# Performance work log

Hardware: AMD Instinct MI355X
Metric: run time of the kernel (lower is better)

The kernel has to match this reference:

```python
import jax, jax.numpy as jnp
import numpy as np

HEADS = 16
KEY_SIZE = 64
SIZE_PER_HEAD = 64
D_MODEL = 1024
OUT_DIM = HEADS * SIZE_PER_HEAD
NEG_BIG = 1e10


def setup_inputs() -> dict:
    key = jax.random.key(0)
    ks = jax.random.split(key, 8)
    B, S = 4, 2048
    q = jax.random.normal(ks[0], (B, S, D_MODEL), dtype=jnp.float32)
    k = jax.random.normal(ks[1], (B, S, D_MODEL), dtype=jnp.float32)
    v = jax.random.normal(ks[2], (B, S, D_MODEL), dtype=jnp.float32)
    # binary masks (1 = keep), as floats like the Keras layer expects
    v_mask = (jax.random.uniform(ks[3], (B, S)) > 0.1).astype(jnp.float32)
    q_mask = (jax.random.uniform(ks[4], (B, S)) > 0.1).astype(jnp.float32)
    sc = 1.0 / np.sqrt(D_MODEL)
    Wq = jax.random.normal(ks[5], (D_MODEL, HEADS * KEY_SIZE), dtype=jnp.float32) * sc
    Wk = jax.random.normal(ks[6], (D_MODEL, HEADS * KEY_SIZE), dtype=jnp.float32) * sc
    Wv = jax.random.normal(ks[7], (D_MODEL, OUT_DIM), dtype=jnp.float32) * sc
    return {"q": q, "k": k, "v": v, "v_mask": v_mask, "q_mask": q_mask,
            "Wq": Wq, "Wk": Wk, "Wv": Wv}


def reference(q, k, v, v_mask, q_mask, Wq, Wk, Wv):
    B, Sq, _ = q.shape
    Sk = k.shape[1]
    # projections -> [B, H, S, d]
    qw = (q @ Wq).reshape(B, Sq, HEADS, KEY_SIZE).transpose(0, 2, 1, 3)
    kw = (k @ Wk).reshape(B, Sk, HEADS, KEY_SIZE).transpose(0, 2, 1, 3)
    vw = (v @ Wv).reshape(B, Sk, HEADS, SIZE_PER_HEAD).transpose(0, 2, 1, 3)
    # scaled scores [B, H, Sq, Sk]
    a = jnp.einsum('bhqd,bhkd->bhqk', qw, kw) / np.sqrt(KEY_SIZE).astype(np.float32)
    # additive key-side mask (v_mask broadcasts over heads and query axis)
    a = a - (1.0 - v_mask[:, None, None, :]) * NEG_BIG
    # causal (mask_right): subtract big value on strictly upper triangle
    causal = jnp.triu(jnp.ones((Sq, Sk), dtype=a.dtype), k=1) * NEG_BIG
    a = a - causal[None, None]
    a = jax.nn.softmax(a, axis=-1)
    o = jnp.einsum('bhqk,bhkd->bhqd', a, vw)
    o = o.transpose(0, 2, 1, 3).reshape(B, Sq, OUT_DIM)
    # multiplicative query-side mask
    o = o * q_mask[:, :, None]
    return o
```

## Files before the change

kernel.cpp:

```cpp
#include <hip/hip_runtime.h>
#include <hip/hip_bf16.h>

typedef __bf16 bf16x8 __attribute__((ext_vector_type(8)));
typedef float f32x4 __attribute__((ext_vector_type(4)));
typedef unsigned int u32;

#define MFMA16(a, b, c) __builtin_amdgcn_mfma_f32_16x16x32_bf16(a, b, c, 0, 0, 0)

static __device__ __forceinline__ unsigned short f2b(float f) {
    __hip_bfloat16 b = __float2bfloat16(f);
    return __builtin_bit_cast(unsigned short, b);
}
static __device__ __forceinline__ float b2f(unsigned short u) {
    u32 v = ((u32)u) << 16;
    return __builtin_bit_cast(float, v);
}
static __device__ __forceinline__ unsigned short f2b_trunc(float f) {
    return (unsigned short)(__builtin_bit_cast(u32, f) >> 16);
}
static __device__ __forceinline__ void glds16(const void* g, void* l) {
    __builtin_amdgcn_global_load_lds((const __attribute__((address_space(1))) u32*)g,
                                     (__attribute__((address_space(3))) u32*)l, 16, 0, 0);
}

__global__ __launch_bounds__(256) void cvt_kernel(const float* __restrict__ src,
                                                  unsigned short* __restrict__ dst) {
    const size_t i = ((size_t)blockIdx.x * 256 + threadIdx.x) * 8;
    float4 a = *(const float4*)(src + i);
    float4 b = *(const float4*)(src + i + 4);
    ushort4 u0 = { f2b(a.x), f2b(a.y), f2b(a.z), f2b(a.w) };
    ushort4 u1 = { f2b(b.x), f2b(b.y), f2b(b.z), f2b(b.w) };
    *(ushort4*)(dst + i) = u0;
    *(ushort4*)(dst + i + 4) = u1;
}

__global__ void wt_kernel(const float* __restrict__ W0, const float* __restrict__ W1,
                          const float* __restrict__ W2, unsigned short* __restrict__ T0,
                          unsigned short* __restrict__ T1, unsigned short* __restrict__ T2) {
    const float* W = blockIdx.z == 0 ? W0 : (blockIdx.z == 1 ? W1 : W2);
    unsigned short* T = blockIdx.z == 0 ? T0 : (blockIdx.z == 1 ? T1 : T2);
    __shared__ float tile[32][33];
    const int n0 = blockIdx.x * 32, k0 = blockIdx.y * 32;
    const int tx = threadIdx.x, ty = threadIdx.y;
#pragma unroll
    for (int i = 0; i < 4; i++)
        tile[ty + 8 * i][tx] = W[(size_t)(k0 + ty + 8 * i) * 1024 + n0 + tx];
    __syncthreads();
#pragma unroll
    for (int i = 0; i < 4; i++)
        T[(size_t)(n0 + ty + 8 * i) * 1024 + k0 + tx] = f2b(tile[tx][ty + 8 * i]);
}

__global__ __launch_bounds__(256) void proj_kernel(const unsigned short* __restrict__ A,
        const unsigned short* __restrict__ Wt, unsigned short* __restrict__ dst,
        const int vmode) {
    __shared__ unsigned short smem[17408];
    unsigned short* As = smem;
    unsigned short* Bs = smem + 4096;
    const int m0 = blockIdx.y * 128, n0 = blockIdx.x * 128;
    const int tid = threadIdx.x;
    const int w = tid >> 6, lane = tid & 63, quad = lane >> 4, l16 = lane & 15;
    const int wr = (w >> 1) * 64, wc = (w & 1) * 64;
    f32x4 acc[4][4] = {};
    for (int kb = 0; kb < 32; kb++) {
        const int k0 = kb * 32;
        __syncthreads();
#pragma unroll
        for (int i = 0; i < 2; i++) {
            int idx = tid + i * 256;
            int row = idx >> 2, col = (idx & 3) * 8;
            glds16(A + (size_t)(m0 + row) * 1024 + k0 + col, &As[idx * 8]);
            glds16(Wt + (size_t)(n0 + row) * 1024 + k0 + col, &Bs[idx * 8]);
        }
        __syncthreads();
        bf16x8 af[4], bf[4];
#pragma unroll
        for (int mt = 0; mt < 4; mt++) af[mt] = *(const bf16x8*)&As[(wr + mt * 16 + l16) * 32 + quad * 8];
#pragma unroll
        for (int nt = 0; nt < 4; nt++) bf[nt] = *(const bf16x8*)&Bs[(wc + nt * 16 + l16) * 32 + quad * 8];
#pragma unroll
        for (int mt = 0; mt < 4; mt++)
#pragma unroll
            for (int nt = 0; nt < 4; nt++)
                acc[mt][nt] = MFMA16(af[mt], bf[nt], acc[mt][nt]);
    }
    __syncthreads();
    unsigned short* Tw = smem + w * 4352;
    if (vmode == 0) {
#pragma unroll
        for (int mt = 0; mt < 4; mt++)
#pragma unroll
            for (int nt = 0; nt < 4; nt++)
#pragma unroll
                for (int r = 0; r < 4; r++)
                    Tw[(mt * 16 + quad * 4 + r) * 68 + nt * 16 + l16] = f2b(acc[mt][nt][r]);
    } else {
#pragma unroll
        for (int mt = 0; mt < 4; mt++)
#pragma unroll
            for (int nt = 0; nt < 4; nt++)
#pragma unroll
                for (int r = 0; r < 4; r++)
                    Tw[(nt * 16 + l16) * 68 + mt * 16 + quad * 4 + r] = f2b(acc[mt][nt][r]);
    }
    const int gr0 = m0 + wr, gc0 = n0 + wc;
    const int b = gr0 >> 11, s0 = gr0 & 2047, h = gc0 >> 6;
    if (vmode == 0) {
        const size_t obase = (size_t)(b * 16 + h) * 2048;
#pragma unroll
        for (int j = 0; j < 16; j++) {
            int row = j * 4 + quad;
            uint2 val = *(const uint2*)&Tw[row * 68 + l16 * 4];
            *(uint2*)(dst + (obase + s0 + row) * 64 + l16 * 4) = val;
        }
    } else {
        const size_t vbase = (size_t)(b * 16 + h) * 64 * 2048;
#pragma unroll
        for (int j = 0; j < 16; j++) {
            int row = j * 4 + quad;
            uint2 val = *(const uint2*)&Tw[row * 68 + l16 * 4];
            *(uint2*)(dst + vbase + (size_t)row * 2048 + s0 + l16 * 4) = val;
        }
    }
}

__global__ __launch_bounds__(256) void attn_kernel(
        const unsigned short* __restrict__ Qp, const unsigned short* __restrict__ Kp,
        const unsigned short* __restrict__ Vt, const float* __restrict__ vmask,
        const float* __restrict__ qmask, float* __restrict__ out) {
    __shared__ unsigned short Ks[4096];
    __shared__ unsigned short Vts[4096];
    __shared__ unsigned short Ps[4096];
    __shared__ float Vmb[2048];
    const int bh = blockIdx.y, b = bh >> 4, h = bh & 15;
    const int tid = threadIdx.x;
    const int w = tid >> 6, lane = tid & 63, quad = lane >> 4, l16 = lane & 15;
    const size_t base = (size_t)bh * 2048 * 64;
    const float C1 = 0.18033688f;
    const float C0 = -11.54156036f;
    const float CM = -1.44269504e10f;
    for (int i = tid; i < 2048; i += 256)
        Vmb[i] = (vmask[b * 2048 + i] != 0.f) ? C0 : (C0 + CM);

    for (int pass = 0; pass < 2; pass++) {
        const int qt = pass ? 31 - blockIdx.x : blockIdx.x;
        const int q0 = qt * 64;
        bf16x8 qa[2];
#pragma unroll
        for (int ks = 0; ks < 2; ks++)
            qa[ks] = *(const bf16x8*)(Qp + base +
                (size_t)(q0 + w * 16 + l16) * 64 + ks * 32 + quad * 8);
        f32x4 o[4] = {};
        float lsum[4] = {};
        const int qrow = q0 + w * 16 + quad * 4;

        for (int kt = 0; kt <= qt; kt++) {
            __syncthreads();
#pragma unroll
            for (int i = 0; i < 2; i++) {
                int idx = tid + i * 256;
                int chunk = idx & 3, row = (idx >> 2) & 63, panel = idx >> 8;
                glds16(Kp + base + (size_t)(kt * 64 + row) * 64 + panel * 32 + chunk * 8, &Ks[idx * 8]);
                glds16(Vt + base + (size_t)row * 2048 + kt * 64 + panel * 32 + chunk * 8, &Vts[idx * 8]);
            }
            __syncthreads();

            f32x4 s[4];
#pragma unroll
            for (int nt = 0; nt < 4; nt++) {
                bf16x8 kf0 = *(const bf16x8*)&Ks[(nt * 16 + l16) * 32 + quad * 8];
                bf16x8 kf1 = *(const bf16x8*)&Ks[2048 + (nt * 16 + l16) * 32 + quad * 8];
                f32x4 z = {};
                z = MFMA16(qa[0], kf0, z);
                z = MFMA16(qa[1], kf1, z);
                s[nt] = z;
            }
#pragma unroll
            for (int nt = 0; nt < 4; nt++) {
                const int kv = kt * 64 + nt * 16 + l16;
                const float cb = Vmb[kv];
#pragma unroll
                for (int r = 0; r < 4; r++) {
                    float p = __builtin_amdgcn_exp2f(s[nt][r] * C1 + cb);
                    p = (kv > qrow + r) ? 0.f : p;
                    lsum[r] += p;
                    Ps[(nt >> 1) * 2048 + (w * 16 + quad * 4 + r) * 32 + (nt & 1) * 16 + l16] = f2b_trunc(p);
                }
            }
#pragma unroll
            for (int k2 = 0; k2 < 2; k2++) {
                bf16x8 pa = *(const bf16x8*)&Ps[k2 * 2048 + (w * 16 + l16) * 32 + quad * 8];
#pragma unroll
                for (int dt = 0; dt < 4; dt++) {
                    bf16x8 vb = *(const bf16x8*)&Vts[k2 * 2048 + (dt * 16 + l16) * 32 + quad * 8];
                    o[dt] = MFMA16(pa, vb, o[dt]);
                }
            }
        }
        float l[4];
#pragma unroll
        for (int r = 0; r < 4; r++) {
            float t = lsum[r];
#pragma unroll
            for (int off = 1; off < 16; off <<= 1) t += __shfl_xor(t, off);
            l[r] = t;
        }
        bool deg = (l[0] == 0.f) | (l[1] == 0.f) | (l[2] == 0.f) | (l[3] == 0.f);
        if (__any((int)deg)) {
#pragma unroll
            for (int r = 0; r < 4; r++)
                if (l[r] == 0.f) {
                    const int qr = qrow + r;
                    float cnt = 0.f;
                    float oacc[4] = {0.f, 0.f, 0.f, 0.f};
                    for (int kv = 0; kv < 2048; kv++) {
                        bool keep = (kv <= qr) || (vmask[b * 2048 + kv] != 0.f);
                        if (keep) {
                            cnt += 1.f;
#pragma unroll
                            for (int dt = 0; dt < 4; dt++)
                                oacc[dt] += b2f(Vt[base + (size_t)(dt * 16 + l16) * 2048 + kv]);
                        }
                    }
                    l[r] = cnt;
#pragma unroll
                    for (int dt = 0; dt < 4; dt++) o[dt][r] = oacc[dt];
                }
        }
#pragma unroll
        for (int r = 0; r < 4; r++) {
            int q = qrow + r;
            float sc = qmask[b * 2048 + q] / l[r];
#pragma unroll
            for (int dt = 0; dt < 4; dt++)
                out[(size_t)(b * 2048 + q) * 1024 + h * 64 + dt * 16 + l16] = o[dt][r] * sc;
        }
    }
}

extern "C" void kernel_launch(void* const* d_in, const int* in_sizes, int n_in,
                              void* d_out, int out_size, void* d_ws, size_t ws_size,
                              hipStream_t stream) {
    const float* q  = (const float*)d_in[0];
    const float* k  = (const float*)d_in[1];
    const float* v  = (const float*)d_in[2];
    const float* vm = (const float*)d_in[3];
    const float* qm = (const float*)d_in[4];
    const float* Wq = (const float*)d_in[5];
    const float* Wk = (const float*)d_in[6];
    const float* Wv = (const float*)d_in[7];
    float* out = (float*)d_out;

    unsigned short* ws  = (unsigned short*)d_ws;
    unsigned short* Wtq = ws;
    unsigned short* Wtk = Wtq + (1u << 20);
    unsigned short* Wtv = Wtk + (1u << 20);
    unsigned short* Qp  = Wtv + (1u << 20);
    unsigned short* Kp  = Qp + (1u << 23);
    unsigned short* Vtp = Kp + (1u << 23);
    unsigned short* Acvt = (unsigned short*)d_out;

    wt_kernel<<<dim3(32, 32, 3), dim3(32, 8), 0, stream>>>(Wq, Wk, Wv, Wtq, Wtk, Wtv);
    cvt_kernel<<<4096, 256, 0, stream>>>(q, Acvt);
    proj_kernel<<<dim3(8, 64), 256, 0, stream>>>(Acvt, Wtq, Qp, 0);
    cvt_kernel<<<4096, 256, 0, stream>>>(k, Acvt);
    proj_kernel<<<dim3(8, 64), 256, 0, stream>>>(Acvt, Wtk, Kp, 0);
    cvt_kernel<<<4096, 256, 0, stream>>>(v, Acvt);
    proj_kernel<<<dim3(8, 64), 256, 0, stream>>>(Acvt, Wtv, Vtp, 1);
    attn_kernel<<<dim3(16, 64), 256, 0, stream>>>(Qp, Kp, Vtp, vm, qm, out);
}
```

Measured before the change: 329.8 us.

## Batch Q/K projections, deepen GEMM K-tile, keep P in registers in attention

Q and K conversion and projection are batched into single launches with a z/y grid dimension, and the projection GEMM loads a 64-wide K slab per barrier pair, halving barrier count. Attention computes S transposed so the probabilities land directly in the MFMA A-operand layout, removing the LDS round trip for P. The causal mask is applied only on the diagonal tile, and K/V load addresses are precomputed. Grid axes are swapped so blocks of the same head are adjacent. The cost is more LDS per projection block and a dependence on the MFMA register layout being correct.

```diff
diff --git a/kernel.cpp b/kernel.cpp
--- a/kernel.cpp
+++ b/kernel.cpp
@@ -4,6 +4,7 @@
 typedef __bf16 bf16x8 __attribute__((ext_vector_type(8)));
 typedef float f32x4 __attribute__((ext_vector_type(4)));
 typedef unsigned int u32;
+typedef u32 u32x4 __attribute__((ext_vector_type(4)));
 
 #define MFMA16(a, b, c) __builtin_amdgcn_mfma_f32_16x16x32_bf16(a, b, c, 0, 0, 0)
 
@@ -15,16 +16,19 @@
     u32 v = ((u32)u) << 16;
     return __builtin_bit_cast(float, v);
 }
-static __device__ __forceinline__ unsigned short f2b_trunc(float f) {
-    return (unsigned short)(__builtin_bit_cast(u32, f) >> 16);
+static __device__ __forceinline__ u32 pk2(float lo, float hi) {
+    return (__builtin_bit_cast(u32, lo) >> 16) | (__builtin_bit_cast(u32, hi) & 0xFFFF0000u);
 }
 static __device__ __forceinline__ void glds16(const void* g, void* l) {
     __builtin_amdgcn_global_load_lds((const __attribute__((address_space(1))) u32*)g,
                                      (__attribute__((address_space(3))) u32*)l, 16, 0, 0);
 }
 
-__global__ __launch_bounds__(256) void cvt_kernel(const float* __restrict__ src,
-                                                  unsigned short* __restrict__ dst) {
+__global__ __launch_bounds__(256) void cvt2_kernel(const float* __restrict__ s0,
+        const float* __restrict__ s1, unsigned short* __restrict__ d0,
+        unsigned short* __restrict__ d1) {
+    const float* src = blockIdx.y ? s1 : s0;
+    unsigned short* dst = blockIdx.y ? d1 : d0;
     const size_t i = ((size_t)blockIdx.x * 256 + threadIdx.x) * 8;
     float4 a = *(const float4*)(src + i);
     float4 b = *(const float4*)(src + i + 4);
@@ -51,38 +55,54 @@
         T[(size_t)(n0 + ty + 8 * i) * 1024 + k0 + tx] = f2b(tile[tx][ty + 8 * i]);
 }
 
-__global__ __launch_bounds__(256) void proj_kernel(const unsigned short* __restrict__ A,
-        const unsigned short* __restrict__ Wt, unsigned short* __restrict__ dst,
-        const int vmode) {
+__global__ __launch_bounds__(256) void proj_kernel(
+        const unsigned short* __restrict__ A0, const unsigned short* __restrict__ A1,
+        const unsigned short* __restrict__ W0, const unsigned short* __restrict__ W1,
+        unsigned short* __restrict__ D0, unsigned short* __restrict__ D1, const int vmode) {
     __shared__ unsigned short smem[17408];
     unsigned short* As = smem;
-    unsigned short* Bs = smem + 4096;
-    const int m0 = blockIdx.y * 128, n0 = blockIdx.x * 128;
+    unsigned short* Bs = smem + 8192;
+    const unsigned short* A  = blockIdx.z ? A1 : A0;
+    const unsigned short* Wt = blockIdx.z ? W1 : W0;
+    unsigned short* dst      = blockIdx.z ? D1 : D0;
+    const int m0 = blockIdx.x * 128, n0 = blockIdx.y * 128;
     const int tid = threadIdx.x;
     const int w = tid >> 6, lane = tid & 63, quad = lane >> 4, l16 = lane & 15;
     const int wr = (w >> 1) * 64, wc = (w & 1) * 64;
+    const unsigned short* ap[4];
+    const unsigned short* bp[4];
+#pragma unroll
+    for (int i = 0; i < 4; i++) {
+        int idx = tid + i * 256;
+        int row = (idx >> 2) & 127, ch = (idx >> 9) * 4 + (idx & 3);
+        ap[i] = A + (size_t)(m0 + row) * 1024 + ch * 8;
+        bp[i] = Wt + (size_t)(n0 + row) * 1024 + ch * 8;
+    }
     f32x4 acc[4][4] = {};
-    for (int kb = 0; kb < 32; kb++) {
-        const int k0 = kb * 32;
+    for (int kb = 0; kb < 16; kb++) {
         __syncthreads();
 #pragma unroll
-        for (int i = 0; i < 2; i++) {
-            int idx = tid + i * 256;
-            int row = idx >> 2, col = (idx & 3) * 8;
-            glds16(A + (size_t)(m0 + row) * 1024 + k0 + col, &As[idx * 8]);
-            glds16(Wt + (size_t)(n0 + row) * 1024 + k0 + col, &Bs[idx * 8]);
+        for (int i = 0; i < 4; i++) {
+            glds16(ap[i], &As[(tid + i * 256) * 8]);
+            glds16(bp[i], &Bs[(tid + i * 256) * 8]);
+            ap[i] += 64; bp[i] += 64;
         }
         __syncthreads();
-        bf16x8 af[4], bf[4];
-#pragma unroll
-        for (int mt = 0; mt < 4; mt++) af[mt] = *(const bf16x8*)&As[(wr + mt * 16 + l16) * 32 + quad * 8];
-#pragma unroll
-        for (int nt = 0; nt < 4; nt++) bf[nt] = *(const bf16x8*)&Bs[(wc + nt * 16 + l16) * 32 + quad * 8];
-#pragma unroll
-        for (int mt = 0; mt < 4; mt++)
+#pragma unroll
+        for (int kp = 0; kp < 2; kp++) {
+            bf16x8 af[4], bf[4];
+#pragma unroll
+            for (int mt = 0; mt < 4; mt++)
+                af[mt] = *(const bf16x8*)&As[kp * 4096 + (wr + mt * 16 + l16) * 32 + quad * 8];
 #pragma unroll
             for (int nt = 0; nt < 4; nt++)
-                acc[mt][nt] = MFMA16(af[mt], bf[nt], acc[mt][nt]);
+                bf[nt] = *(const bf16x8*)&Bs[kp * 4096 + (wc + nt * 16 + l16) * 32 + quad * 8];
+#pragma unroll
+            for (int mt = 0; mt < 4; mt++)
+#pragma unroll
+                for (int nt = 0; nt < 4; nt++)
+                    acc[mt][nt] = MFMA16(af[mt], bf[nt], acc[mt][nt]);
+        }
     }
     __syncthreads();
     unsigned short* Tw = smem + w * 4352;
@@ -130,9 +150,8 @@
         const float* __restrict__ qmask, float* __restrict__ out) {
     __shared__ unsigned short Ks[4096];
     __shared__ unsigned short Vts[4096];
-    __shared__ unsigned short Ps[4096];
     __shared__ float Vmb[2048];
-    const int bh = blockIdx.y, b = bh >> 4, h = bh & 15;
+    const int bh = blockIdx.x, b = bh >> 4, h = bh & 15;
     const int tid = threadIdx.x;
     const int w = tid >> 6, lane = tid & 63, quad = lane >> 4, l16 = lane & 15;
     const size_t base = (size_t)bh * 2048 * 64;
@@ -142,8 +161,14 @@
     for (int i = tid; i < 2048; i += 256)
         Vmb[i] = (vmask[b * 2048 + i] != 0.f) ? C0 : (C0 + CM);
 
+    const int i0 = tid, i1 = tid + 256;
+    const unsigned short* kp0 = Kp + base + (size_t)((i0 >> 2) & 63) * 64 + (i0 >> 8) * 32 + (i0 & 3) * 8;
+    const unsigned short* kp1 = Kp + base + (size_t)((i1 >> 2) & 63) * 64 + (i1 >> 8) * 32 + (i1 & 3) * 8;
+    const unsigned short* vp0 = Vt + base + (size_t)((i0 >> 2) & 63) * 2048 + (i0 >> 8) * 32 + (i0 & 3) * 8;
+    const unsigned short* vp1 = Vt + base + (size_t)((i1 >> 2) & 63) * 2048 + (i1 >> 8) * 32 + (i1 & 3) * 8;
+
     for (int pass = 0; pass < 2; pass++) {
-        const int qt = pass ? 31 - blockIdx.x : blockIdx.x;
+        const int qt = pass ? 31 - blockIdx.y : blockIdx.y;
         const int q0 = qt * 64;
         bf16x8 qa[2];
 #pragma unroll
@@ -151,66 +176,69 @@
             qa[ks] = *(const bf16x8*)(Qp + base +
                 (size_t)(q0 + w * 16 + l16) * 64 + ks * 32 + quad * 8);
         f32x4 o[4] = {};
-        float lsum[4] = {};
-        const int qrow = q0 + w * 16 + quad * 4;
-
-        for (int kt = 0; kt <= qt; kt++) {
+        float lsum = 0.f;
+
+        auto do_tile = [&](int kt, bool diag) __attribute__((always_inline)) {
             __syncthreads();
-#pragma unroll
-            for (int i = 0; i < 2; i++) {
-                int idx = tid + i * 256;
-                int chunk = idx & 3, row = (idx >> 2) & 63, panel = idx >> 8;
-                glds16(Kp + base + (size_t)(kt * 64 + row) * 64 + panel * 32 + chunk * 8, &Ks[idx * 8]);
-                glds16(Vt + base + (size_t)row * 2048 + kt * 64 + panel * 32 + chunk * 8, &Vts[idx * 8]);
-            }
+            glds16(kp0 + (size_t)kt * 4096, &Ks[i0 * 8]);
+            glds16(kp1 + (size_t)kt * 4096, &Ks[i1 * 8]);
+            glds16(vp0 + kt * 64, &Vts[i0 * 8]);
+            glds16(vp1 + kt * 64, &Vts[i1 * 8]);
             __syncthreads();
 
-            f32x4 s[4];
+            f32x4 st[4];
 #pragma unroll
             for (int nt = 0; nt < 4; nt++) {
                 bf16x8 kf0 = *(const bf16x8*)&Ks[(nt * 16 + l16) * 32 + quad * 8];
                 bf16x8 kf1 = *(const bf16x8*)&Ks[2048 + (nt * 16 + l16) * 32 + quad * 8];
                 f32x4 z = {};
-                z = MFMA16(qa[0], kf0, z);
-                z = MFMA16(qa[1], kf1, z);
-                s[nt] = z;
+                z = MFMA16(kf0, qa[0], z);
+                z = MFMA16(kf1, qa[1], z);
+                st[nt] = z;
             }
+            float p[4][4];
 #pragma unroll
             for (int nt = 0; nt < 4; nt++) {
-                const int kv = kt * 64 + nt * 16 + l16;
-                const float cb = Vmb[kv];
+                f32x4 vb4 = *(const f32x4*)&Vmb[kt * 64 + nt * 16 + quad * 4];
 #pragma unroll
                 for (int r = 0; r < 4; r++) {
-                    float p = __builtin_amdgcn_exp2f(s[nt][r] * C1 + cb);
-                    p = (kv > qrow + r) ? 0.f : p;
-                    lsum[r] += p;
-                    Ps[(nt >> 1) * 2048 + (w * 16 + quad * 4 + r) * 32 + (nt & 1) * 16 + l16] = f2b_trunc(p);
+                    float pv = __builtin_amdgcn_exp2f(st[nt][r] * C1 + vb4[r]);
+                    if (diag)
+                        pv = (nt * 16 + quad * 4 + r > w * 16 + l16) ? 0.f : pv;
+                    p[nt][r] = pv;
+                    lsum += pv;
                 }
             }
 #pragma unroll
-            for (int k2 = 0; k2 < 2; k2++) {
-                bf16x8 pa = *(const bf16x8*)&Ps[k2 * 2048 + (w * 16 + l16) * 32 + quad * 8];
+            for (int h2 = 0; h2 < 2; h2++) {
+                u32x4 pw = { pk2(p[2 * h2][0], p[2 * h2][1]), pk2(p[2 * h2][2], p[2 * h2][3]),
+                             pk2(p[2 * h2 + 1][0], p[2 * h2 + 1][1]), pk2(p[2 * h2 + 1][2], p[2 * h2 + 1][3]) };
+                bf16x8 pa = __builtin_bit_cast(bf16x8, pw);
 #pragma unroll
                 for (int dt = 0; dt < 4; dt++) {
-                    bf16x8 vb = *(const bf16x8*)&Vts[k2 * 2048 + (dt * 16 + l16) * 32 + quad * 8];
-                    o[dt] = MFMA16(pa, vb, o[dt]);
+                    const unsigned short* vp = &Vts[h2 * 2048 + (dt * 16 + l16) * 32 + quad * 4];
+                    uint2 v0 = *(const uint2*)vp;
+                    uint2 v1 = *(const uint2*)(vp + 16);
+                    u32x4 vw = { v0.x, v0.y, v1.x, v1.y };
+                    o[dt] = MFMA16(pa, __builtin_bit_cast(bf16x8, vw), o[dt]);
                 }
             }
-        }
-        float l[4];
-#pragma unroll
-        for (int r = 0; r < 4; r++) {
-            float t = lsum[r];
-#pragma unroll
-            for (int off = 1; off < 16; off <<= 1) t += __shfl_xor(t, off);
-            l[r] = t;
-        }
-        bool deg = (l[0] == 0.f) | (l[1] == 0.f) | (l[2] == 0.f) | (l[3] == 0.f);
+        };
+        for (int kt = 0; kt < qt; kt++) do_tile(kt, false);
+        do_tile(qt, true);
+
+        float lf = lsum;
+        lf += __shfl_xor(lf, 16);
+        lf += __shfl_xor(lf, 32);
+        float lr[4];
+#pragma unroll
+        for (int r = 0; r < 4; r++) lr[r] = __shfl(lf, quad * 4 + r);
+        bool deg = (lr[0] == 0.f) | (lr[1] == 0.f) | (lr[2] == 0.f) | (lr[3] == 0.f);
         if (__any((int)deg)) {
 #pragma unroll
             for (int r = 0; r < 4; r++)
-                if (l[r] == 0.f) {
-                    const int qr = qrow + r;
+                if (lr[r] == 0.f) {
+                    const int qr = q0 + w * 16 + quad * 4 + r;
                     float cnt = 0.f;
                     float oacc[4] = {0.f, 0.f, 0.f, 0.f};
                     for (int kv = 0; kv < 2048; kv++) {
@@ -222,15 +250,15 @@
                                 oacc[dt] += b2f(Vt[base + (size_t)(dt * 16 + l16) * 2048 + kv]);
                         }
                     }
-                    l[r] = cnt;
+                    lr[r] = cnt;
 #pragma unroll
                     for (int dt = 0; dt < 4; dt++) o[dt][r] = oacc[dt];
                 }
         }
 #pragma unroll
         for (int r = 0; r < 4; r++) {
-            int q = qrow + r;
-            float sc = qmask[b * 2048 + q] / l[r];
+            int q = q0 + w * 16 + quad * 4 + r;
+            float sc = qmask[b * 2048 + q] / lr[r];
 #pragma unroll
             for (int dt = 0; dt < 4; dt++)
                 out[(size_t)(b * 2048 + q) * 1024 + h * 64 + dt * 16 + l16] = o[dt][r] * sc;
@@ -258,14 +286,13 @@
     unsigned short* Qp  = Wtv + (1u << 20);
     unsigned short* Kp  = Qp + (1u << 23);
     unsigned short* Vtp = Kp + (1u << 23);
-    unsigned short* Acvt = (unsigned short*)d_out;
+    unsigned short* Aq = (unsigned short*)d_out;
+    unsigned short* Ak = Aq + (1u << 23);
 
     wt_kernel<<<dim3(32, 32, 3), dim3(32, 8), 0, stream>>>(Wq, Wk, Wv, Wtq, Wtk, Wtv);
-    cvt_kernel<<<4096, 256, 0, stream>>>(q, Acvt);
-    proj_kernel<<<dim3(8, 64), 256, 0, stream>>>(Acvt, Wtq, Qp, 0);
-    cvt_kernel<<<4096, 256, 0, stream>>>(k, Acvt);
-    proj_kernel<<<dim3(8, 64), 256, 0, stream>>>(Acvt, Wtk, Kp, 0);
-    cvt_kernel<<<4096, 256, 0, stream>>>(v, Acvt);
-    proj_kernel<<<dim3(8, 64), 256, 0, stream>>>(Acvt, Wtv, Vtp, 1);
-    attn_kernel<<<dim3(16, 64), 256, 0, stream>>>(Qp, Kp, Vtp, vm, qm, out);
-}
+    cvt2_kernel<<<dim3(4096, 2), 256, 0, stream>>>(q, k, Aq, Ak);
+    proj_kernel<<<dim3(64, 8, 2), 256, 0, stream>>>(Aq, Ak, Wtq, Wtk, Qp, Kp, 0);
+    cvt2_kernel<<<dim3(4096, 1), 256, 0, stream>>>(v, v, Aq, Aq);
+    proj_kernel<<<dim3(64, 8, 1), 256, 0, stream>>>(Aq, Aq, Wtv, Wtv, Vtp, Vtp, 1);
+    attn_kernel<<<dim3(64, 16), 256, 0, stream>>>(Qp, Kp, Vtp, vm, qm, out);
+}
```

After: 361.3 us. 1.1x slower.
